# Performance work log

Measured on AMD Instinct MI355X. Metric: run time of the kernel, lower is better.

Reference implementation:

```python
import jax, jax.numpy as jnp
import numpy as np

LN_EPS = 1e-10


def _log_g(x):
    # log of g(x) where g(x) = x + 0.5 for x >= 0 else sigmoid(x)
    return jnp.where(x >= 0, jnp.log(jax.nn.relu(x) + 0.5), -jax.nn.softplus(-x))


def setup_inputs() -> dict:
    key = jax.random.key(0)
    k1, k2 = jax.random.split(key)
    B, T, D, H = 8, 4096, 512, 512
    x = jax.random.normal(k1, (B, T, D), dtype=jnp.float32)
    ln_gamma = jnp.ones((D,), dtype=jnp.float32)
    ln_beta = jnp.zeros((D,), dtype=jnp.float32)
    W_gh = jax.random.normal(k2, (D, 2 * H), dtype=jnp.float32) * 0.02
    return {"x": x, "ln_gamma": ln_gamma, "ln_beta": ln_beta, "W_gh": W_gh}


def reference(x, ln_gamma, ln_beta, W_gh):
    # LayerNorm over last dim
    mu = jnp.mean(x, axis=-1, keepdims=True)
    var = jnp.mean(jnp.square(x - mu), axis=-1, keepdims=True)
    xn = (x - mu) * jax.lax.rsqrt(var + LN_EPS) * ln_gamma + ln_beta

    # minGRU projection: gate logits k and candidate pre-activation
    gh = jnp.einsum('btd,dh->bth', xn, W_gh)  # [B, T, 2H]
    H = W_gh.shape[1] // 2
    k_gate, h_pre = gh[..., :H], gh[..., H:]

    # log-space parallel scan (Heinsen): h_t = (1-z_t) h_{t-1} + z_t g(h_pre_t)
    log_z = -jax.nn.softplus(-k_gate)        # log sigmoid(k)
    log_coeffs = -jax.nn.softplus(k_gate)    # log(1 - sigmoid(k))
    log_values = log_z + _log_g(h_pre)

    a_star = jnp.cumsum(log_coeffs, axis=1)
    log_h = a_star + jax.lax.cumlogsumexp(log_values - a_star, axis=1)
    h = jnp.exp(log_h)  # [B, T, H]

    # residual (res_proj is Identity since input_size == hidden_size)
    out = h + x
    hidden = h[:, -1]  # last hidden state [B, H]
    return out, hidden
```

## Files before the change

### kernel.cpp

```cpp
#include <hip/hip_runtime.h>
#include <stdint.h>

#define NB 8
#define NT 4096
#define ND 512
#define NH 512
#define NN 1024
#define NM (NB * NT)
#define NK 512
#define NCH 128
#define CTS 32

typedef __bf16 bf16x8 __attribute__((ext_vector_type(8)));
typedef float floatx4 __attribute__((ext_vector_type(4)));
typedef unsigned int uint_g __attribute__((address_space(1)));
typedef unsigned int uint_l __attribute__((address_space(3)));

__device__ __forceinline__ float bf2f(unsigned short u) {
    union { unsigned int i; float f; } v; v.i = ((unsigned int)u) << 16; return v.f;
}
__device__ __forceinline__ unsigned short f2bf(float f) {
    union { float f; unsigned int i; } v; v.f = f;
    return (unsigned short)((v.i + 0x7FFFu + ((v.i >> 16) & 1u)) >> 16);
}

__device__ __forceinline__ void load_lds16(const void* g, void* l) {
    __builtin_amdgcn_global_load_lds((const uint_g*)g, (uint_l*)l, 16, 0, 0);
}

__global__ __launch_bounds__(256) void ln_kernel(const float* __restrict__ x,
                                                 const float* __restrict__ gamma,
                                                 const float* __restrict__ beta,
                                                 unsigned short* __restrict__ xn) {
    int wid = threadIdx.x >> 6, lane = threadIdx.x & 63;
    size_t row = (size_t)blockIdx.x * 4 + wid;
    const float4* xr = (const float4*)(x + row * ND);
    float4 v0 = xr[lane];
    float4 v1 = xr[lane + 64];
    float s  = (v0.x + v0.y) + (v0.z + v0.w) + (v1.x + v1.y) + (v1.z + v1.w);
    float sq = v0.x * v0.x + v0.y * v0.y + v0.z * v0.z + v0.w * v0.w
             + v1.x * v1.x + v1.y * v1.y + v1.z * v1.z + v1.w * v1.w;
#pragma unroll
    for (int off = 32; off > 0; off >>= 1) {
        s  += __shfl_xor(s,  off, 64);
        sq += __shfl_xor(sq, off, 64);
    }
    float mu   = s * (1.0f / ND);
    float var  = sq * (1.0f / ND) - mu * mu;
    float rstd = rsqrtf(var + 1e-10f);
    const float4* gr = (const float4*)gamma;
    const float4* br = (const float4*)beta;
    float4 g0 = gr[lane], g1 = gr[lane + 64];
    float4 b0 = br[lane], b1 = br[lane + 64];
    ushort4 o0, o1;
    o0.x = f2bf((v0.x - mu) * rstd * g0.x + b0.x);
    o0.y = f2bf((v0.y - mu) * rstd * g0.y + b0.y);
    o0.z = f2bf((v0.z - mu) * rstd * g0.z + b0.z);
    o0.w = f2bf((v0.w - mu) * rstd * g0.w + b0.w);
    o1.x = f2bf((v1.x - mu) * rstd * g1.x + b1.x);
    o1.y = f2bf((v1.y - mu) * rstd * g1.y + b1.y);
    o1.z = f2bf((v1.z - mu) * rstd * g1.z + b1.z);
    o1.w = f2bf((v1.w - mu) * rstd * g1.w + b1.w);
    ushort4* xo = (ushort4*)(xn + row * ND);
    xo[lane]      = o0;
    xo[lane + 64] = o1;
}

__global__ __launch_bounds__(256) void wt_kernel(const float* __restrict__ W,
                                                 unsigned short* __restrict__ Wt) {
    __shared__ float tile[32][33];
    int n0 = blockIdx.x * 32;
    int k0 = blockIdx.y * 32;
    int tx = threadIdx.x, ty = threadIdx.y;
#pragma unroll
    for (int j = 0; j < 4; ++j)
        tile[ty + j * 8][tx] = W[(size_t)(k0 + ty + j * 8) * NN + n0 + tx];
    __syncthreads();
#pragma unroll
    for (int j = 0; j < 4; ++j)
        Wt[(size_t)(n0 + ty + j * 8) * NK + k0 + tx] = f2bf(tile[tx][ty + j * 8]);
}

__global__ __launch_bounds__(256) void gemm_kernel(const unsigned short* __restrict__ A,
                                                   const unsigned short* __restrict__ Bt,
                                                   unsigned short* __restrict__ C) {
    __shared__ __align__(16) unsigned short As[128 * 64];
    __shared__ __align__(16) unsigned short Bs[128 * 64];
    int tid  = threadIdx.x;
    int lane = tid & 63;
    int wid  = tid >> 6;
    int wm = wid & 1, wn = wid >> 1;
    int bx = blockIdx.x;
    int nt = bx & 7;
    int mt = bx >> 3;
    const int Rm = mt * 128, Rn = nt * 128;

    int rloc = lane >> 3;
    int cl   = lane & 7;
    int cg   = cl ^ rloc;

    int frow = lane & 15;
    int quad = lane >> 4;
    int fx   = lane & 7;

    floatx4 acc[4][4];
#pragma unroll
    for (int i = 0; i < 4; ++i)
#pragma unroll
        for (int j = 0; j < 4; ++j)
            acc[i][j] = (floatx4){0.f, 0.f, 0.f, 0.f};

#pragma unroll 1
    for (int kt = 0; kt < NK / 64; ++kt) {
        int k0 = kt * 64;
        __syncthreads();
#pragma unroll
        for (int s = 0; s < 4; ++s) {
            int g  = wid * 4 + s;
            int ml = g * 8 + rloc;
            load_lds16(A + (size_t)(Rm + ml) * NK + k0 + cg * 8, As + g * 512);
        }
#pragma unroll
        for (int s = 0; s < 4; ++s) {
            int g  = wid * 4 + s;
            int nl = g * 8 + rloc;
            load_lds16(Bt + (size_t)(Rn + nl) * NK + k0 + cg * 8, Bs + g * 512);
        }
        __syncthreads();
#pragma unroll
        for (int ks = 0; ks < 2; ++ks) {
            int ch = (ks * 4 + quad) ^ fx;
            bf16x8 af[4], bfr[4];
#pragma unroll
            for (int mi = 0; mi < 4; ++mi) {
                int ml = wm * 64 + mi * 16 + frow;
                af[mi] = *(const bf16x8*)(As + ml * 64 + ch * 8);
            }
#pragma unroll
            for (int ni = 0; ni < 4; ++ni) {
                int nl = wn * 64 + ni * 16 + frow;
                bfr[ni] = *(const bf16x8*)(Bs + nl * 64 + ch * 8);
            }
#pragma unroll
            for (int mi = 0; mi < 4; ++mi)
#pragma unroll
                for (int ni = 0; ni < 4; ++ni)
                    acc[mi][ni] = __builtin_amdgcn_mfma_f32_16x16x32_bf16(
                        af[mi], bfr[ni], acc[mi][ni], 0, 0, 0);
        }
    }
#pragma unroll
    for (int mi = 0; mi < 4; ++mi)
#pragma unroll
        for (int ni = 0; ni < 4; ++ni)
#pragma unroll
            for (int r = 0; r < 4; ++r) {
                int row = Rm + wm * 64 + mi * 16 + quad * 4 + r;
                int col = Rn + wn * 64 + ni * 16 + frow;
                C[(size_t)row * NN + col] = f2bf(acc[mi][ni][r]);
            }
}

__device__ __forceinline__ void gate_av(unsigned short ku, unsigned short pu,
                                        float& a, float& v) {
    float k = bf2f(ku), p = bf2f(pu);
    float e = __expf(k);
    a = __builtin_amdgcn_rcpf(1.0f + e);
    float z = e * a;
    float gneg = __builtin_amdgcn_rcpf(1.0f + __expf(-p));
    float g = (p >= 0.0f) ? (p + 0.5f) : gneg;
    v = z * g;
}

__global__ __launch_bounds__(128) void scan1_kernel(const unsigned short* __restrict__ gh,
                                                    float* __restrict__ cA,
                                                    float* __restrict__ cV) {
    int b = blockIdx.x >> 7, c = blockIdx.x & 127;
    int h = threadIdx.x * 4;
    const unsigned short* base = gh + ((size_t)(b * NT + c * CTS)) * NN;
    float A0 = 1.f, A1 = 1.f, A2 = 1.f, A3 = 1.f;
    float V0 = 0.f, V1 = 0.f, V2 = 0.f, V3 = 0.f;
#pragma unroll 8
    for (int t = 0; t < CTS; ++t) {
        const unsigned short* p = base + (size_t)t * NN;
        ushort4 kk = *(const ushort4*)(p + h);
        ushort4 hh = *(const ushort4*)(p + NH + h);
        float a, v;
        gate_av(kk.x, hh.x, a, v); V0 = a * V0 + v; A0 *= a;
        gate_av(kk.y, hh.y, a, v); V1 = a * V1 + v; A1 *= a;
        gate_av(kk.z, hh.z, a, v); V2 = a * V2 + v; A2 *= a;
        gate_av(kk.w, hh.w, a, v); V3 = a * V3 + v; A3 *= a;
    }
    size_t o = ((size_t)b * NH + h) * NCH + c;
    cA[o] = A0; cA[o + NCH] = A1; cA[o + 2 * NCH] = A2; cA[o + 3 * NCH] = A3;
    cV[o] = V0; cV[o + NCH] = V1; cV[o + 2 * NCH] = V2; cV[o + 3 * NCH] = V3;
}

__global__ __launch_bounds__(256) void scan2_kernel(const float* __restrict__ cA,
                                                    const float* __restrict__ cV,
                                                    float* __restrict__ hinit) {
    int w = blockIdx.x * 4 + (threadIdx.x >> 6);
    int lane = threadIdx.x & 63;
    int b = w >> 9, h = w & 511;
    const float2* a2p = (const float2*)(cA + ((size_t)b * NH + h) * NCH);
    const float2* v2p = (const float2*)(cV + ((size_t)b * NH + h) * NCH);
    float2 a2 = a2p[lane];
    float2 v2 = v2p[lane];
    float A = a2.y * a2.x;
    float V = a2.y * v2.x + v2.y;
#pragma unroll
    for (int off = 1; off < 64; off <<= 1) {
        float Ap = __shfl_up(A, off, 64);
        float Vp = __shfl_up(V, off, 64);
        if (lane >= off) { V = A * Vp + V; A = A * Ap; }
    }
    float excl = __shfl_up(V, 1, 64);
    if (lane == 0) excl = 0.f;
    float e0 = excl;
    float e1 = a2.x * e0 + v2.x;
    hinit[((size_t)b * NCH + 2 * lane) * NH + h]     = e0;
    hinit[((size_t)b * NCH + 2 * lane + 1) * NH + h] = e1;
}

__global__ __launch_bounds__(128) void scan3_kernel(const unsigned short* __restrict__ gh,
                                                    const float* __restrict__ hinit,
                                                    const float* __restrict__ x,
                                                    float* __restrict__ out,
                                                    float* __restrict__ hidden) {
    int b = blockIdx.x >> 7, c = blockIdx.x & 127;
    int h = threadIdx.x * 4;
    size_t row0 = (size_t)(b * NT + c * CTS);
    const unsigned short* base = gh + row0 * NN;
    const float* xb = x + row0 * ND;
    float* ob = out + row0 * ND;
    float4 hv = *(const float4*)(hinit + ((size_t)b * NCH + c) * NH + h);
#pragma unroll 8
    for (int t = 0; t < CTS; ++t) {
        const unsigned short* p = base + (size_t)t * NN;
        ushort4 kk = *(const ushort4*)(p + h);
        ushort4 hh = *(const ushort4*)(p + NH + h);
        float a, v;
        gate_av(kk.x, hh.x, a, v); hv.x = a * hv.x + v;
        gate_av(kk.y, hh.y, a, v); hv.y = a * hv.y + v;
        gate_av(kk.z, hh.z, a, v); hv.z = a * hv.z + v;
        gate_av(kk.w, hh.w, a, v); hv.w = a * hv.w + v;
        float4 xv = *(const float4*)(xb + (size_t)t * ND + h);
        float4 ov;
        ov.x = hv.x + xv.x; ov.y = hv.y + xv.y;
        ov.z = hv.z + xv.z; ov.w = hv.w + xv.w;
        *(float4*)(ob + (size_t)t * ND + h) = ov;
    }
    if (c == NCH - 1)
        *(float4*)(hidden + (size_t)b * NH + h) = hv;
}

extern "C" void kernel_launch(void* const* d_in, const int* in_sizes, int n_in,
                              void* d_out, int out_size, void* d_ws, size_t ws_size,
                              hipStream_t stream) {
    const float* x     = (const float*)d_in[0];
    const float* gamma = (const float*)d_in[1];
    const float* beta  = (const float*)d_in[2];
    const float* W     = (const float*)d_in[3];

    float* out    = (float*)d_out;
    float* hidden = out + (size_t)NM * ND;

    char* ws = (char*)d_ws;
    unsigned short* Wt = (unsigned short*)ws;
    unsigned short* gh = (unsigned short*)(ws + (size_t)(1u << 20));
    float* cA    = (float*)(ws + (size_t)(1u << 20) + (size_t)NM * NN * 2);
    float* cV    = cA + (size_t)NB * NCH * NH;
    float* hinit = cV + (size_t)NB * NCH * NH;
    unsigned short* xn = (unsigned short*)d_out;

    wt_kernel<<<dim3(32, 16), dim3(32, 8), 0, stream>>>(W, Wt);
    ln_kernel<<<NM / 4, 256, 0, stream>>>(x, gamma, beta, xn);
    gemm_kernel<<<2048, 256, 0, stream>>>(xn, Wt, gh);
    scan1_kernel<<<NB * NCH, 128, 0, stream>>>(gh, cA, cV);
    scan2_kernel<<<1024, 256, 0, stream>>>(cA, cV, hinit);
    scan3_kernel<<<NB * NCH, 128, 0, stream>>>(gh, hinit, x, out, hidden);
}
```

Baseline: 231.8 us.

## Merge weight transpose into LayerNorm launch, reorder GEMM tiles, batch scan loads

Folds the weight transpose/convert kernel into the LayerNorm kernel as extra blocks, removing one launch. The GEMM block mapping is changed so consecutive blocks walk M tiles for a fixed N tile rather than N tiles for a fixed M tile, which changes L2 reuse of the A and B operands. Both scan kernels now issue eight timesteps of loads up front before doing the recurrence, to raise memory-level parallelism at the cost of more registers.

After: 215.8 us. -6.9%, faster.

```diff
diff --git a/kernel.cpp b/kernel.cpp
--- a/kernel.cpp
+++ b/kernel.cpp
@@ -28,12 +28,29 @@
     __builtin_amdgcn_global_load_lds((const uint_g*)g, (uint_l*)l, 16, 0, 0);
 }
 
-__global__ __launch_bounds__(256) void ln_kernel(const float* __restrict__ x,
-                                                 const float* __restrict__ gamma,
-                                                 const float* __restrict__ beta,
-                                                 unsigned short* __restrict__ xn) {
+__global__ __launch_bounds__(256) void prep_kernel(const float* __restrict__ x,
+                                                   const float* __restrict__ gamma,
+                                                   const float* __restrict__ beta,
+                                                   const float* __restrict__ W,
+                                                   unsigned short* __restrict__ xn,
+                                                   unsigned short* __restrict__ Wt) {
+    if (blockIdx.x < 512) {
+        __shared__ float tile[32][33];
+        int bid = blockIdx.x;
+        int n0 = (bid & 31) * 32;
+        int k0 = (bid >> 5) * 32;
+        int tx = threadIdx.x & 31, ty = threadIdx.x >> 5;
+#pragma unroll
+        for (int j = 0; j < 4; ++j)
+            tile[ty + j * 8][tx] = W[(size_t)(k0 + ty + j * 8) * NN + n0 + tx];
+        __syncthreads();
+#pragma unroll
+        for (int j = 0; j < 4; ++j)
+            Wt[(size_t)(n0 + ty + j * 8) * NK + k0 + tx] = f2bf(tile[tx][ty + j * 8]);
+        return;
+    }
     int wid = threadIdx.x >> 6, lane = threadIdx.x & 63;
-    size_t row = (size_t)blockIdx.x * 4 + wid;
+    size_t row = (size_t)(blockIdx.x - 512) * 4 + wid;
     const float4* xr = (const float4*)(x + row * ND);
     float4 v0 = xr[lane];
     float4 v1 = xr[lane + 64];
@@ -66,21 +83,6 @@
     xo[lane + 64] = o1;
 }
 
-__global__ __launch_bounds__(256) void wt_kernel(const float* __restrict__ W,
-                                                 unsigned short* __restrict__ Wt) {
-    __shared__ float tile[32][33];
-    int n0 = blockIdx.x * 32;
-    int k0 = blockIdx.y * 32;
-    int tx = threadIdx.x, ty = threadIdx.y;
-#pragma unroll
-    for (int j = 0; j < 4; ++j)
-        tile[ty + j * 8][tx] = W[(size_t)(k0 + ty + j * 8) * NN + n0 + tx];
-    __syncthreads();
-#pragma unroll
-    for (int j = 0; j < 4; ++j)
-        Wt[(size_t)(n0 + ty + j * 8) * NK + k0 + tx] = f2bf(tile[tx][ty + j * 8]);
-}
-
 __global__ __launch_bounds__(256) void gemm_kernel(const unsigned short* __restrict__ A,
                                                    const unsigned short* __restrict__ Bt,
                                                    unsigned short* __restrict__ C) {
@@ -91,8 +93,8 @@
     int wid  = tid >> 6;
     int wm = wid & 1, wn = wid >> 1;
     int bx = blockIdx.x;
-    int nt = bx & 7;
-    int mt = bx >> 3;
+    int mt = bx & 255;
+    int nt = bx >> 8;
     const int Rm = mt * 128, Rn = nt * 128;
 
     int rloc = lane >> 3;
@@ -177,19 +179,26 @@
                                                     float* __restrict__ cV) {
     int b = blockIdx.x >> 7, c = blockIdx.x & 127;
     int h = threadIdx.x * 4;
-    const unsigned short* base = gh + ((size_t)(b * NT + c * CTS)) * NN;
+    const unsigned short* base = gh + ((size_t)(b * NT + c * CTS)) * NN + h;
     float A0 = 1.f, A1 = 1.f, A2 = 1.f, A3 = 1.f;
     float V0 = 0.f, V1 = 0.f, V2 = 0.f, V3 = 0.f;
-#pragma unroll 8
-    for (int t = 0; t < CTS; ++t) {
-        const unsigned short* p = base + (size_t)t * NN;
-        ushort4 kk = *(const ushort4*)(p + h);
-        ushort4 hh = *(const ushort4*)(p + NH + h);
-        float a, v;
-        gate_av(kk.x, hh.x, a, v); V0 = a * V0 + v; A0 *= a;
-        gate_av(kk.y, hh.y, a, v); V1 = a * V1 + v; A1 *= a;
-        gate_av(kk.z, hh.z, a, v); V2 = a * V2 + v; A2 *= a;
-        gate_av(kk.w, hh.w, a, v); V3 = a * V3 + v; A3 *= a;
+#pragma unroll 1
+    for (int tb = 0; tb < CTS; tb += 8) {
+        ushort4 kb[8], hb[8];
+#pragma unroll
+        for (int j = 0; j < 8; ++j) {
+            const unsigned short* p = base + (size_t)(tb + j) * NN;
+            kb[j] = *(const ushort4*)p;
+            hb[j] = *(const ushort4*)(p + NH);
+        }
+#pragma unroll
+        for (int j = 0; j < 8; ++j) {
+            float a, v;
+            gate_av(kb[j].x, hb[j].x, a, v); V0 = a * V0 + v; A0 *= a;
+            gate_av(kb[j].y, hb[j].y, a, v); V1 = a * V1 + v; A1 *= a;
+            gate_av(kb[j].z, hb[j].z, a, v); V2 = a * V2 + v; A2 *= a;
+            gate_av(kb[j].w, hb[j].w, a, v); V3 = a * V3 + v; A3 *= a;
+        }
     }
     size_t o = ((size_t)b * NH + h) * NCH + c;
     cA[o] = A0; cA[o + NCH] = A1; cA[o + 2 * NCH] = A2; cA[o + 3 * NCH] = A3;
@@ -230,25 +239,33 @@
     int b = blockIdx.x >> 7, c = blockIdx.x & 127;
     int h = threadIdx.x * 4;
     size_t row0 = (size_t)(b * NT + c * CTS);
-    const unsigned short* base = gh + row0 * NN;
-    const float* xb = x + row0 * ND;
-    float* ob = out + row0 * ND;
+    const unsigned short* base = gh + row0 * NN + h;
+    const float* xb = x + row0 * ND + h;
+    float* ob = out + row0 * ND + h;
     float4 hv = *(const float4*)(hinit + ((size_t)b * NCH + c) * NH + h);
-#pragma unroll 8
-    for (int t = 0; t < CTS; ++t) {
-        const unsigned short* p = base + (size_t)t * NN;
-        ushort4 kk = *(const ushort4*)(p + h);
-        ushort4 hh = *(const ushort4*)(p + NH + h);
-        float a, v;
-        gate_av(kk.x, hh.x, a, v); hv.x = a * hv.x + v;
-        gate_av(kk.y, hh.y, a, v); hv.y = a * hv.y + v;
-        gate_av(kk.z, hh.z, a, v); hv.z = a * hv.z + v;
-        gate_av(kk.w, hh.w, a, v); hv.w = a * hv.w + v;
-        float4 xv = *(const float4*)(xb + (size_t)t * ND + h);
-        float4 ov;
-        ov.x = hv.x + xv.x; ov.y = hv.y + xv.y;
-        ov.z = hv.z + xv.z; ov.w = hv.w + xv.w;
-        *(float4*)(ob + (size_t)t * ND + h) = ov;
+#pragma unroll 1
+    for (int tb = 0; tb < CTS; tb += 8) {
+        ushort4 kb[8], hb[8];
+        float4 xv[8];
+#pragma unroll
+        for (int j = 0; j < 8; ++j) {
+            const unsigned short* p = base + (size_t)(tb + j) * NN;
+            kb[j] = *(const ushort4*)p;
+            hb[j] = *(const ushort4*)(p + NH);
+            xv[j] = *(const float4*)(xb + (size_t)(tb + j) * ND);
+        }
+#pragma unroll
+        for (int j = 0; j < 8; ++j) {
+            float a, v;
+            gate_av(kb[j].x, hb[j].x, a, v); hv.x = a * hv.x + v;
+            gate_av(kb[j].y, hb[j].y, a, v); hv.y = a * hv.y + v;
+            gate_av(kb[j].z, hb[j].z, a, v); hv.z = a * hv.z + v;
+            gate_av(kb[j].w, hb[j].w, a, v); hv.w = a * hv.w + v;
+            float4 ov;
+            ov.x = hv.x + xv[j].x; ov.y = hv.y + xv[j].y;
+            ov.z = hv.z + xv[j].z; ov.w = hv.w + xv[j].w;
+            *(float4*)(ob + (size_t)(tb + j) * ND) = ov;
+        }
     }
     if (c == NCH - 1)
         *(float4*)(hidden + (size_t)b * NH + h) = hv;
@@ -273,8 +290,7 @@
     float* hinit = cV + (size_t)NB * NCH * NH;
     unsigned short* xn = (unsigned short*)d_out;
 
-    wt_kernel<<<dim3(32, 16), dim3(32, 8), 0, stream>>>(W, Wt);
-    ln_kernel<<<NM / 4, 256, 0, stream>>>(x, gamma, beta, xn);
+    prep_kernel<<<512 + NM / 4, 256, 0, stream>>>(x, gamma, beta, W, xn, Wt);
     gemm_kernel<<<2048, 256, 0, stream>>>(xn, Wt, gh);
     scan1_kernel<<<NB * NCH, 128, 0, stream>>>(gh, cA, cV);
     scan2_kernel<<<1024, 256, 0, stream>>>(cA, cV, hinit);
```
